# Performance work log

Measured on AMD Instinct MI355X. Metric: run time of the kernel, lower is better.

Reference implementation:

```python
import jax, jax.numpy as jnp
import numpy as np

M, K = 3072, 768          # hardcoded in the torch module's forward
B, S = 8, 2048            # batch, sequence length
NNZ_PER_ROW = 230
NNZ = M * NNZ_PER_ROW


def setup_inputs() -> dict:
    key = jax.random.key(0)
    k1, k2, k3 = jax.random.split(key, 3)
    rng = np.random.default_rng(0)
    # unique, sorted column indices per row (valid CSR with fixed row nnz)
    cols = np.argsort(rng.random((M, K)), axis=1)[:, :NNZ_PER_ROW]
    cols = np.sort(cols, axis=1).astype(np.int32)
    column_indices = jnp.asarray(cols.reshape(-1))
    row_offsets = jnp.asarray((np.arange(M + 1) * NNZ_PER_ROW).astype(np.int32))
    # diffsort(row_offsets): rows sorted by nnz descending (all equal -> identity)
    row_indices = jnp.arange(M, dtype=jnp.int32)
    values = jax.random.normal(k1, (NNZ,), dtype=jnp.float32) * 0.02
    bias = jax.random.normal(k2, (M,), dtype=jnp.float32) * 0.02
    x = jax.random.normal(k3, (B, S, K), dtype=jnp.float32)
    return {"values": values, "bias": bias, "x": x,
            "row_indices": row_indices, "row_offsets": row_offsets,
            "column_indices": column_indices}


def reference(values, bias, x, row_indices, row_offsets, column_indices):
    # CSR [M, K] sparse weight times dense x: out = x @ W^T + bias
    # (left_spmm(m,k,...,x^T) gives [B, M, S]; .transpose(1,2) -> [B, S, M])
    nnz = values.shape[0]
    # row id of each nonzero from the CSR offsets
    row_ids = jnp.searchsorted(row_offsets, jnp.arange(nnz, dtype=row_offsets.dtype), side="right") - 1
    # scatter values into the (small) dense [M, K] weight; .add sums duplicates
    # exactly as SpMM accumulation would
    W = jnp.zeros((M, K), dtype=values.dtype).at[row_ids, column_indices].add(values)
    out = jnp.einsum("bsk,mk->bsm", x, W) + bias  # [B, S, M]
    return out
```

## Files before the change

### kernel.cpp

```cpp
#include <hip/hip_runtime.h>
#include <hip/hip_bf16.h>
#include <cstdint>

#define K_DIM 768
#define M_DIM 3072
#define BS_TOTAL 16384
#define KT 12

typedef __attribute__((ext_vector_type(4))) float f32x4;
typedef __attribute__((ext_vector_type(8))) short bf16x8;
typedef __attribute__((ext_vector_type(4))) unsigned short u16x4;
typedef __attribute__((ext_vector_type(4))) float fv4;

typedef unsigned int u32_g __attribute__((address_space(1)));
typedef unsigned int u32_l __attribute__((address_space(3)));

static __device__ __forceinline__ void async_load16(const void* g, void* l) {
    __builtin_amdgcn_global_load_lds((const u32_g*)g, (u32_l*)l, 16, 0, 0);
}

#define BAR() __builtin_amdgcn_s_barrier()
#define SCHEDB() __builtin_amdgcn_sched_barrier(0)

static __device__ __forceinline__ unsigned short f2bf(float f) {
    unsigned u = __builtin_bit_cast(unsigned, f);
    u += 0x7fffu + ((u >> 16) & 1u);
    return (unsigned short)(u >> 16);
}

__global__ void prep_kernel(const float* __restrict__ values,
                            const int* __restrict__ row_offsets,
                            const int* __restrict__ column_indices,
                            unsigned short* __restrict__ Wb,
                            const float* __restrict__ x,
                            unsigned short* __restrict__ xb, int n4) {
    const int b = blockIdx.x;
    const int t = threadIdx.x;
    if (b < M_DIM) {
        const int r = b;
        unsigned int* wrow32 = (unsigned int*)(Wb + (size_t)r * K_DIM);
        for (int i = t; i < K_DIM / 2; i += 256) wrow32[i] = 0u;
        __syncthreads();
        const int start = row_offsets[r], end = row_offsets[r + 1];
        unsigned short* wrow = Wb + (size_t)r * K_DIM;
        for (int i = start + t; i < end; i += 256)
            wrow[column_indices[i]] = f2bf(values[i]);
    } else {
        const int i = (b - M_DIM) * 256 + t;
        if (i < n4) {
            fv4 v = ((const fv4*)x)[i];
            u16x4 o;
            o[0] = f2bf(v[0]); o[1] = f2bf(v[1]); o[2] = f2bf(v[2]); o[3] = f2bf(v[3]);
            ((u16x4*)xb)[i] = o;
        }
    }
}


#define STAGE_A(buf, t, half)                                                   \
    { _Pragma("unroll") for (int c = 0; c < 2; ++c) {                           \
        const int u = c * 512 + tid;                                            \
        const int row = (half) * 128 + (u >> 3);                                \
        const int gs = (u & 7) ^ (row & 7);                                     \
        async_load16(X + (size_t)(row0 + row) * K_DIM + (t) * 64 + gs * 8,      \
                     &sm[buf][0][row * 64 + (u & 7) * 8]); } }

#define STAGE_B(buf, t, half)                                                   \
    { _Pragma("unroll") for (int c = 0; c < 2; ++c) {                           \
        const int u = c * 512 + tid;                                            \
        const int row = (half) * 128 + (u >> 3);                                \
        const int gs = (u & 7) ^ (row & 7);                                     \
        async_load16(W + (size_t)(col0 + row) * K_DIM + (t) * 64 + gs * 8,      \
                     &sm[buf][1][row * 64 + (u & 7) * 8]); } }

#define LDA(buf, mh)                                                            \
    { _Pragma("unroll") for (int mi = 0; mi < 4; ++mi) {                        \
        const int row = wm * 128 + (mh) * 64 + mi * 16 + fr;                    \
        const int sw = (row & 7) << 3;                                          \
        aq[mi][0] = *(const bf16x8*)&sm[buf][0][row * 64 + ((kq * 8) ^ sw)];    \
        aq[mi][1] = *(const bf16x8*)&sm[buf][0][row * 64 + ((32 + kq * 8) ^ sw)]; } }

#define LDB(buf, nh, breg)                                                      \
    { _Pragma("unroll") for (int ni = 0; ni < 2; ++ni) {                        \
        const int row = wn * 64 + (nh) * 32 + ni * 16 + fr;                     \
        const int sw = (row & 7) << 3;                                          \
        breg[ni][0] = *(const bf16x8*)&sm[buf][1][row * 64 + ((kq * 8) ^ sw)];  \
        breg[ni][1] = *(const bf16x8*)&sm[buf][1][row * 64 + ((32 + kq * 8) ^ sw)]; } }

#define MFMA16(mh, nh, breg)                                                    \
    { _Pragma("unroll") for (int mi = 0; mi < 4; ++mi)                          \
      _Pragma("unroll") for (int ni = 0; ni < 2; ++ni) {                        \
        acc[(mh)*4+mi][(nh)*2+ni] = __builtin_amdgcn_mfma_f32_16x16x32_bf16(    \
            aq[mi][0], breg[ni][0], acc[(mh)*4+mi][(nh)*2+ni], 0, 0, 0);        \
        acc[(mh)*4+mi][(nh)*2+ni] = __builtin_amdgcn_mfma_f32_16x16x32_bf16(    \
            aq[mi][1], breg[ni][1], acc[(mh)*4+mi][(nh)*2+ni], 0, 0, 0); } }

__global__ __launch_bounds__(512, 2) void gemm_kernel(
    const unsigned short* __restrict__ X,
    const unsigned short* __restrict__ W,
    const float* __restrict__ bias,
    float* __restrict__ out) {
    __shared__ __align__(16) unsigned short sm[2][2][256 * 64];

    const int bid = blockIdx.x;
    const int xcd = bid & 7;
    const int j   = bid >> 3;
    const int by  = xcd * 8 + (j & 7);
    const int bx  = j >> 3;
    const int row0 = by * 256;
    const int col0 = bx * 256;

    const int tid  = threadIdx.x;
    const int lane = tid & 63;
    const int wave = tid >> 6;
    const int wm = wave >> 2;
    const int wn = wave & 3;
    const int fr = lane & 15;
    const int kq = lane >> 4;

    f32x4 acc[8][4] = {};
    bf16x8 aq[4][2], b0[2][2], b1[2][2];

    STAGE_A(0, 0, 0); STAGE_A(0, 0, 1);
    STAGE_B(0, 0, 0); STAGE_B(0, 0, 1);
    STAGE_B(1, 1, 0); STAGE_B(1, 1, 1);
    asm volatile("s_waitcnt vmcnt(4)" ::: "memory");
    SCHEDB();
    BAR();

    for (int t = 0; t < KT; ++t) {
        const int buf = t & 1, nbuf = buf ^ 1;

        LDA(buf, 0);
        LDB(buf, 0, b0);
        LDB(buf, 1, b1);
        if (t + 1 < KT) { STAGE_A(nbuf, t + 1, 0); STAGE_A(nbuf, t + 1, 1); }
        BAR();
        __builtin_amdgcn_s_setprio(1);
        MFMA16(0, 0, b0);
        MFMA16(0, 1, b1);
        __builtin_amdgcn_s_setprio(0);

        LDA(buf, 1);
        BAR();
        if (t + 2 < KT) { STAGE_B(buf, t + 2, 0); STAGE_B(buf, t + 2, 1); }
        __builtin_amdgcn_s_setprio(1);
        MFMA16(1, 1, b1);
        MFMA16(1, 0, b0);
        __builtin_amdgcn_s_setprio(0);

        if (t + 2 < KT)      { asm volatile("s_waitcnt vmcnt(4)" ::: "memory"); SCHEDB(); BAR(); }
        else if (t + 1 < KT) { asm volatile("s_waitcnt vmcnt(0)" ::: "memory"); SCHEDB(); BAR(); }
    }

    float bv[4];
#pragma unroll
    for (int ni = 0; ni < 4; ++ni) bv[ni] = bias[col0 + wn * 64 + ni * 16 + fr];

    const int orow0 = row0 + wm * 128 + kq * 4;
#pragma unroll
    for (int mi = 0; mi < 8; ++mi)
#pragma unroll
        for (int jj = 0; jj < 4; ++jj) {
            float* op = out + (size_t)(orow0 + mi * 16 + jj) * M_DIM + col0 + wn * 64 + fr;
#pragma unroll
            for (int ni = 0; ni < 4; ++ni)
                op[ni * 16] = acc[mi][ni][jj] + bv[ni];
        }
}

extern "C" void kernel_launch(void* const* d_in, const int* in_sizes, int n_in,
                              void* d_out, int out_size, void* d_ws, size_t ws_size,
                              hipStream_t stream) {
    const float* values         = (const float*)d_in[0];
    const float* bias           = (const float*)d_in[1];
    const float* x              = (const float*)d_in[2];
    const int*   row_offsets    = (const int*)d_in[4];
    const int*   column_indices = (const int*)d_in[5];

    unsigned short* Wb = (unsigned short*)d_ws;
    unsigned short* Xb = (unsigned short*)((char*)d_ws + (size_t)M_DIM * K_DIM * 2);

    const int n4 = BS_TOTAL * K_DIM / 4;
    const int prep_blocks = M_DIM + (n4 + 255) / 256;
    prep_kernel<<<prep_blocks, 256, 0, stream>>>(values, row_offsets, column_indices,
                                                 Wb, x, Xb, n4);

    const int grid = (BS_TOTAL / 256) * (M_DIM / 256);
    gemm_kernel<<<grid, 512, 0, stream>>>(Xb, Wb, bias, (float*)d_out);
}
```

Before: 102.7 us.

## Fuse fp32-to-bf16 conversion of x into GEMM A-tile loading

```diff
diff --git a/kernel.cpp b/kernel.cpp
--- a/kernel.cpp
+++ b/kernel.cpp
@@ -9,7 +9,7 @@
 
 typedef __attribute__((ext_vector_type(4))) float f32x4;
 typedef __attribute__((ext_vector_type(8))) short bf16x8;
-typedef __attribute__((ext_vector_type(4))) unsigned short u16x4;
+typedef __attribute__((ext_vector_type(2))) unsigned int u32x2;
 typedef __attribute__((ext_vector_type(4))) float fv4;
 
 typedef unsigned int u32_g __attribute__((address_space(1)));
@@ -28,42 +28,46 @@
     return (unsigned short)(u >> 16);
 }
 
+static __device__ __forceinline__ unsigned int pack2bf(float a, float b) {
+    unsigned ua = __builtin_bit_cast(unsigned, a);
+    unsigned ub = __builtin_bit_cast(unsigned, b);
+    ua += 0x7fffu + ((ua >> 16) & 1u);
+    ub += 0x7fffu + ((ub >> 16) & 1u);
+    return (ua >> 16) | (ub & 0xffff0000u);
+}
+
 __global__ void prep_kernel(const float* __restrict__ values,
                             const int* __restrict__ row_offsets,
                             const int* __restrict__ column_indices,
-                            unsigned short* __restrict__ Wb,
-                            const float* __restrict__ x,
-                            unsigned short* __restrict__ xb, int n4) {
-    const int b = blockIdx.x;
+                            unsigned short* __restrict__ Wb) {
+    const int r = blockIdx.x;
     const int t = threadIdx.x;
-    if (b < M_DIM) {
-        const int r = b;
-        unsigned int* wrow32 = (unsigned int*)(Wb + (size_t)r * K_DIM);
-        for (int i = t; i < K_DIM / 2; i += 256) wrow32[i] = 0u;
-        __syncthreads();
-        const int start = row_offsets[r], end = row_offsets[r + 1];
-        unsigned short* wrow = Wb + (size_t)r * K_DIM;
-        for (int i = start + t; i < end; i += 256)
-            wrow[column_indices[i]] = f2bf(values[i]);
-    } else {
-        const int i = (b - M_DIM) * 256 + t;
-        if (i < n4) {
-            fv4 v = ((const fv4*)x)[i];
-            u16x4 o;
-            o[0] = f2bf(v[0]); o[1] = f2bf(v[1]); o[2] = f2bf(v[2]); o[3] = f2bf(v[3]);
-            ((u16x4*)xb)[i] = o;
-        }
-    }
-}
-
-
-#define STAGE_A(buf, t, half)                                                   \
-    { _Pragma("unroll") for (int c = 0; c < 2; ++c) {                           \
+    unsigned int* wrow32 = (unsigned int*)(Wb + (size_t)r * K_DIM);
+    for (int i = t; i < K_DIM / 2; i += 256) wrow32[i] = 0u;
+    __syncthreads();
+    const int start = row_offsets[r], end = row_offsets[r + 1];
+    unsigned short* wrow = Wb + (size_t)r * K_DIM;
+    for (int i = start + t; i < end; i += 256)
+        wrow[column_indices[i]] = f2bf(values[i]);
+}
+
+
+#define ALOAD(t)                                                                \
+    { _Pragma("unroll") for (int c = 0; c < 8; ++c) {                           \
         const int u = c * 512 + tid;                                            \
-        const int row = (half) * 128 + (u >> 3);                                \
-        const int gs = (u & 7) ^ (row & 7);                                     \
-        async_load16(X + (size_t)(row0 + row) * K_DIM + (t) * 64 + gs * 8,      \
-                     &sm[buf][0][row * 64 + (u & 7) * 8]); } }
+        const int row = u >> 4, seg = u & 15;                                   \
+        fa[c] = *(const fv4*)(X32 + (size_t)(row0 + row) * K_DIM                \
+                              + (t) * 64 + seg * 4); } }
+
+#define AWRITE(buf)                                                             \
+    { _Pragma("unroll") for (int c = 0; c < 8; ++c) {                           \
+        const int u = c * 512 + tid;                                            \
+        const int row = u >> 4, seg = u & 15;                                   \
+        const int off = row * 64 + (((seg >> 1) ^ (row & 7)) * 8)               \
+                        + (seg & 1) * 4;                                        \
+        u32x2 pk; pk[0] = pack2bf(fa[c][0], fa[c][1]);                          \
+        pk[1] = pack2bf(fa[c][2], fa[c][3]);                                    \
+        *(u32x2*)&smA[buf][off] = pk; } }
 
 #define STAGE_B(buf, t, half)                                                   \
     { _Pragma("unroll") for (int c = 0; c < 2; ++c) {                           \
@@ -71,21 +75,21 @@
         const int row = (half) * 128 + (u >> 3);                                \
         const int gs = (u & 7) ^ (row & 7);                                     \
         async_load16(W + (size_t)(col0 + row) * K_DIM + (t) * 64 + gs * 8,      \
-                     &sm[buf][1][row * 64 + (u & 7) * 8]); } }
+                     &smB[buf][row * 64 + (u & 7) * 8]); } }
 
 #define LDA(buf, mh)                                                            \
     { _Pragma("unroll") for (int mi = 0; mi < 4; ++mi) {                        \
         const int row = wm * 128 + (mh) * 64 + mi * 16 + fr;                    \
         const int sw = (row & 7) << 3;                                          \
-        aq[mi][0] = *(const bf16x8*)&sm[buf][0][row * 64 + ((kq * 8) ^ sw)];    \
-        aq[mi][1] = *(const bf16x8*)&sm[buf][0][row * 64 + ((32 + kq * 8) ^ sw)]; } }
+        aq[mi][0] = *(const bf16x8*)&smA[buf][row * 64 + ((kq * 8) ^ sw)];      \
+        aq[mi][1] = *(const bf16x8*)&smA[buf][row * 64 + ((32 + kq * 8) ^ sw)]; } }
 
 #define LDB(buf, nh, breg)                                                      \
     { _Pragma("unroll") for (int ni = 0; ni < 2; ++ni) {                        \
         const int row = wn * 64 + (nh) * 32 + ni * 16 + fr;                     \
         const int sw = (row & 7) << 3;                                          \
-        breg[ni][0] = *(const bf16x8*)&sm[buf][1][row * 64 + ((kq * 8) ^ sw)];  \
-        breg[ni][1] = *(const bf16x8*)&sm[buf][1][row * 64 + ((32 + kq * 8) ^ sw)]; } }
+        breg[ni][0] = *(const bf16x8*)&smB[buf][row * 64 + ((kq * 8) ^ sw)];    \
+        breg[ni][1] = *(const bf16x8*)&smB[buf][row * 64 + ((32 + kq * 8) ^ sw)]; } }
 
 #define MFMA16(mh, nh, breg)                                                    \
     { _Pragma("unroll") for (int mi = 0; mi < 4; ++mi)                          \
@@ -96,11 +100,12 @@
             aq[mi][1], breg[ni][1], acc[(mh)*4+mi][(nh)*2+ni], 0, 0, 0); } }
 
 __global__ __launch_bounds__(512, 2) void gemm_kernel(
-    const unsigned short* __restrict__ X,
+    const float* __restrict__ X32,
     const unsigned short* __restrict__ W,
     const float* __restrict__ bias,
     float* __restrict__ out) {
-    __shared__ __align__(16) unsigned short sm[2][2][256 * 64];
+    __shared__ __align__(16) unsigned short smA[2][256 * 64];
+    __shared__ __align__(16) unsigned short smB[2][256 * 64];
 
     const int bid = blockIdx.x;
     const int xcd = bid & 7;
@@ -120,12 +125,16 @@
 
     f32x4 acc[8][4] = {};
     bf16x8 aq[4][2], b0[2][2], b1[2][2];
-
-    STAGE_A(0, 0, 0); STAGE_A(0, 0, 1);
+    fv4 fa[8];
+
+    ALOAD(0);
     STAGE_B(0, 0, 0); STAGE_B(0, 0, 1);
     STAGE_B(1, 1, 0); STAGE_B(1, 1, 1);
     asm volatile("s_waitcnt vmcnt(4)" ::: "memory");
     SCHEDB();
+    AWRITE(0);
+    asm volatile("s_waitcnt lgkmcnt(0)" ::: "memory");
+    SCHEDB();
     BAR();
 
     for (int t = 0; t < KT; ++t) {
@@ -134,7 +143,7 @@
         LDA(buf, 0);
         LDB(buf, 0, b0);
         LDB(buf, 1, b1);
-        if (t + 1 < KT) { STAGE_A(nbuf, t + 1, 0); STAGE_A(nbuf, t + 1, 1); }
+        if (t + 1 < KT) ALOAD(t + 1);
         BAR();
         __builtin_amdgcn_s_setprio(1);
         MFMA16(0, 0, b0);
@@ -149,8 +158,15 @@
         MFMA16(1, 0, b0);
         __builtin_amdgcn_s_setprio(0);
 
-        if (t + 2 < KT)      { asm volatile("s_waitcnt vmcnt(4)" ::: "memory"); SCHEDB(); BAR(); }
-        else if (t + 1 < KT) { asm volatile("s_waitcnt vmcnt(0)" ::: "memory"); SCHEDB(); BAR(); }
+        if (t + 1 < KT) {
+            if (t + 2 < KT) { asm volatile("s_waitcnt vmcnt(4)" ::: "memory"); }
+            else            { asm volatile("s_waitcnt vmcnt(0)" ::: "memory"); }
+            SCHEDB();
+            AWRITE(nbuf);
+            asm volatile("s_waitcnt lgkmcnt(0)" ::: "memory");
+            SCHEDB();
+            BAR();
+        }
     }
 
     float bv[4];
@@ -179,13 +195,9 @@
     const int*   column_indices = (const int*)d_in[5];
 
     unsigned short* Wb = (unsigned short*)d_ws;
-    unsigned short* Xb = (unsigned short*)((char*)d_ws + (size_t)M_DIM * K_DIM * 2);
-
-    const int n4 = BS_TOTAL * K_DIM / 4;
-    const int prep_blocks = M_DIM + (n4 + 255) / 256;
-    prep_kernel<<<prep_blocks, 256, 0, stream>>>(values, row_offsets, column_indices,
-                                                 Wb, x, Xb, n4);
+
+    prep_kernel<<<M_DIM, 256, 0, stream>>>(values, row_offsets, column_indices, Wb);
 
     const int grid = (BS_TOTAL / 256) * (M_DIM / 256);
-    gemm_kernel<<<grid, 512, 0, stream>>>(Xb, Wb, bias, (float*)d_out);
-}
+    gemm_kernel<<<grid, 512, 0, stream>>>(x, Wb, bias, (float*)d_out);
+}
```

Result: slower. 182.3 us (+77.4%).

## Prepack weight into MFMA fragment layout and load B directly from global

Applied to the files above, without the earlier changes.

```diff
diff --git a/kernel.cpp b/kernel.cpp
--- a/kernel.cpp
+++ b/kernel.cpp
@@ -31,20 +31,26 @@
 __global__ void prep_kernel(const float* __restrict__ values,
                             const int* __restrict__ row_offsets,
                             const int* __restrict__ column_indices,
-                            unsigned short* __restrict__ Wb,
+                            unsigned short* __restrict__ Wp,
                             const float* __restrict__ x,
                             unsigned short* __restrict__ xb, int n4) {
     const int b = blockIdx.x;
     const int t = threadIdx.x;
     if (b < M_DIM) {
-        const int r = b;
-        unsigned int* wrow32 = (unsigned int*)(Wb + (size_t)r * K_DIM);
-        for (int i = t; i < K_DIM / 2; i += 256) wrow32[i] = 0u;
+        const int r = b, g = r >> 4, fr = r & 15;
+        for (int i = t; i < 96; i += 256) {
+            const int kt = i >> 3, ks = (i >> 2) & 1, kq = i & 3;
+            const int unit = ((kt * 192 + g) * 2 + ks) * 64 + kq * 16 + fr;
+            *(f32x4*)(Wp + (size_t)unit * 8) = (f32x4){0.f, 0.f, 0.f, 0.f};
+        }
         __syncthreads();
         const int start = row_offsets[r], end = row_offsets[r + 1];
-        unsigned short* wrow = Wb + (size_t)r * K_DIM;
-        for (int i = start + t; i < end; i += 256)
-            wrow[column_indices[i]] = f2bf(values[i]);
+        for (int i = start + t; i < end; i += 256) {
+            const int c = column_indices[i];
+            const int kt = c >> 6, ks = (c >> 5) & 1, kq = (c >> 3) & 3, jj = c & 7;
+            const int unit = ((kt * 192 + g) * 2 + ks) * 64 + kq * 16 + fr;
+            Wp[(size_t)unit * 8 + jj] = f2bf(values[i]);
+        }
     } else {
         const int i = (b - M_DIM) * 256 + t;
         if (i < n4) {
@@ -63,29 +69,21 @@
         const int row = (half) * 128 + (u >> 3);                                \
         const int gs = (u & 7) ^ (row & 7);                                     \
         async_load16(X + (size_t)(row0 + row) * K_DIM + (t) * 64 + gs * 8,      \
-                     &sm[buf][0][row * 64 + (u & 7) * 8]); } }
-
-#define STAGE_B(buf, t, half)                                                   \
-    { _Pragma("unroll") for (int c = 0; c < 2; ++c) {                           \
-        const int u = c * 512 + tid;                                            \
-        const int row = (half) * 128 + (u >> 3);                                \
-        const int gs = (u & 7) ^ (row & 7);                                     \
-        async_load16(W + (size_t)(col0 + row) * K_DIM + (t) * 64 + gs * 8,      \
-                     &sm[buf][1][row * 64 + (u & 7) * 8]); } }
+                     &smA[buf][row * 64 + (u & 7) * 8]); } }
 
 #define LDA(buf, mh)                                                            \
     { _Pragma("unroll") for (int mi = 0; mi < 4; ++mi) {                        \
         const int row = wm * 128 + (mh) * 64 + mi * 16 + fr;                    \
         const int sw = (row & 7) << 3;                                          \
-        aq[mi][0] = *(const bf16x8*)&sm[buf][0][row * 64 + ((kq * 8) ^ sw)];    \
-        aq[mi][1] = *(const bf16x8*)&sm[buf][0][row * 64 + ((32 + kq * 8) ^ sw)]; } }
+        aq[mi][0] = *(const bf16x8*)&smA[buf][row * 64 + ((kq * 8) ^ sw)];      \
+        aq[mi][1] = *(const bf16x8*)&smA[buf][row * 64 + ((32 + kq * 8) ^ sw)]; } }
 
-#define LDB(buf, nh, breg)                                                      \
-    { _Pragma("unroll") for (int ni = 0; ni < 2; ++ni) {                        \
-        const int row = wn * 64 + (nh) * 32 + ni * 16 + fr;                     \
-        const int sw = (row & 7) << 3;                                          \
-        breg[ni][0] = *(const bf16x8*)&sm[buf][1][row * 64 + ((kq * 8) ^ sw)];  \
-        breg[ni][1] = *(const bf16x8*)&sm[buf][1][row * 64 + ((32 + kq * 8) ^ sw)]; } }
+#define LDB_G(t, nh, breg)                                                      \
+    { _Pragma("unroll") for (int ni = 0; ni < 2; ++ni)                          \
+      _Pragma("unroll") for (int ks = 0; ks < 2; ++ks) {                        \
+        const int g = colg + wn * 4 + (nh) * 2 + ni;                            \
+        breg[ni][ks] = *(const bf16x8*)(Wp +                                    \
+            (size_t)((((t) * 192 + g) * 2 + ks) * 64 + lane) * 8); } }
 
 #define MFMA16(mh, nh, breg)                                                    \
     { _Pragma("unroll") for (int mi = 0; mi < 4; ++mi)                          \
@@ -97,10 +95,10 @@
 
 __global__ __launch_bounds__(512, 2) void gemm_kernel(
     const unsigned short* __restrict__ X,
-    const unsigned short* __restrict__ W,
+    const unsigned short* __restrict__ Wp,
     const float* __restrict__ bias,
     float* __restrict__ out) {
-    __shared__ __align__(16) unsigned short sm[2][2][256 * 64];
+    __shared__ __align__(16) unsigned short smA[2][256 * 64];
 
     const int bid = blockIdx.x;
     const int xcd = bid & 7;
@@ -108,6 +106,7 @@
     const int by  = xcd * 8 + (j & 7);
     const int bx  = j >> 3;
     const int row0 = by * 256;
+    const int colg = bx * 16;
     const int col0 = bx * 256;
 
     const int tid  = threadIdx.x;
@@ -122,35 +121,36 @@
     bf16x8 aq[4][2], b0[2][2], b1[2][2];
 
     STAGE_A(0, 0, 0); STAGE_A(0, 0, 1);
-    STAGE_B(0, 0, 0); STAGE_B(0, 0, 1);
-    STAGE_B(1, 1, 0); STAGE_B(1, 1, 1);
-    asm volatile("s_waitcnt vmcnt(4)" ::: "memory");
+    asm volatile("s_waitcnt vmcnt(0)" ::: "memory");
     SCHEDB();
     BAR();
 
     for (int t = 0; t < KT; ++t) {
         const int buf = t & 1, nbuf = buf ^ 1;
 
+        LDB_G(t, 0, b0);
+        LDB_G(t, 1, b1);
+        if (t + 1 < KT) { STAGE_A(nbuf, t + 1, 0); STAGE_A(nbuf, t + 1, 1); }
         LDA(buf, 0);
-        LDB(buf, 0, b0);
-        LDB(buf, 1, b1);
-        if (t + 1 < KT) { STAGE_A(nbuf, t + 1, 0); STAGE_A(nbuf, t + 1, 1); }
-        BAR();
+        if (t + 1 < KT) { asm volatile("s_waitcnt vmcnt(4)" ::: "memory"); }
+        else            { asm volatile("s_waitcnt vmcnt(0)" ::: "memory"); }
+        SCHEDB();
+
         __builtin_amdgcn_s_setprio(1);
         MFMA16(0, 0, b0);
         MFMA16(0, 1, b1);
         __builtin_amdgcn_s_setprio(0);
-
         LDA(buf, 1);
-        BAR();
-        if (t + 2 < KT) { STAGE_B(buf, t + 2, 0); STAGE_B(buf, t + 2, 1); }
         __builtin_amdgcn_s_setprio(1);
         MFMA16(1, 1, b1);
         MFMA16(1, 0, b0);
         __builtin_amdgcn_s_setprio(0);
 
-        if (t + 2 < KT)      { asm volatile("s_waitcnt vmcnt(4)" ::: "memory"); SCHEDB(); BAR(); }
-        else if (t + 1 < KT) { asm volatile("s_waitcnt vmcnt(0)" ::: "memory"); SCHEDB(); BAR(); }
+        if (t + 1 < KT) {
+            asm volatile("s_waitcnt vmcnt(0)" ::: "memory");
+            SCHEDB();
+            BAR();
+        }
     }
 
     float bv[4];
@@ -178,14 +178,14 @@
     const int*   row_offsets    = (const int*)d_in[4];
     const int*   column_indices = (const int*)d_in[5];
 
-    unsigned short* Wb = (unsigned short*)d_ws;
+    unsigned short* Wp = (unsigned short*)d_ws;
     unsigned short* Xb = (unsigned short*)((char*)d_ws + (size_t)M_DIM * K_DIM * 2);
 
     const int n4 = BS_TOTAL * K_DIM / 4;
     const int prep_blocks = M_DIM + (n4 + 255) / 256;
     prep_kernel<<<prep_blocks, 256, 0, stream>>>(values, row_offsets, column_indices,
-                                                 Wb, x, Xb, n4);
+                                                 Wp, x, Xb, n4);
 
     const int grid = (BS_TOTAL / 256) * (M_DIM / 256);
-    gemm_kernel<<<grid, 512, 0, stream>>>(Xb, Wb, bias, (float*)d_out);
+    gemm_kernel<<<grid, 512, 0, stream>>>(Xb, Wp, bias, (float*)d_out);
 }
```

After: 120.6 us. 1.17x slower.
